# Optimization experiments

Measured on AMD Instinct MI355X. Metric: run time of the kernel, lower is better.

## Reference

```python
import jax, jax.numpy as jnp
import numpy as np

N_NODES = 50000
N_EDGES = 800000
IN_DIM = 64
EDGE_DIM = 32
OUT_DIM = 64
HID = IN_DIM + EDGE_DIM  # repo MLP defaults hidden width = layer input width


def setup_inputs() -> dict:
    key = jax.random.key(0)
    ks = jax.random.split(key, 7)
    x = jax.random.normal(ks[0], (N_NODES, IN_DIM), dtype=jnp.float32)
    edge_index = jax.random.randint(ks[1], (2, N_EDGES), 0, N_NODES, dtype=jnp.int64)
    edge_attr = jax.random.normal(ks[2], (N_EDGES, EDGE_DIM), dtype=jnp.float32)
    s1 = 1.0 / np.sqrt(HID)
    s2 = 1.0 / np.sqrt(HID)
    W1 = jax.random.normal(ks[3], (HID, HID), dtype=jnp.float32) * s1
    b1 = jnp.zeros((HID,), dtype=jnp.float32)
    W2 = jax.random.normal(ks[4], (HID, OUT_DIM), dtype=jnp.float32) * s2
    b2 = jnp.zeros((OUT_DIM,), dtype=jnp.float32)
    return {"x": x, "edge_index": edge_index, "edge_attr": edge_attr,
            "W1": W1, "b1": b1, "W2": W2, "b2": b2}


def reference(x, edge_index, edge_attr, W1, b1, W2, b2):
    row, col = edge_index[0], edge_index[1]
    n_nodes = x.shape[0]
    # gather source node features and fuse with edge features: [E, IN+EDGE]
    h = jnp.concatenate([x[row], edge_attr], axis=1)
    # MLP: one hidden layer with ReLU, linear output
    h = jax.nn.relu(h @ W1 + b1)
    h = h @ W2 + b2  # [E, OUT_DIM]
    # scatter_mean over destination (col) indices
    summed = jax.ops.segment_sum(h, col, num_segments=n_nodes)  # [N, OUT_DIM]
    counts = jax.ops.segment_sum(jnp.ones((h.shape[0],), dtype=h.dtype), col,
                                 num_segments=n_nodes)
    return summed / jnp.maximum(counts, 1.0)[:, None]
```

## Files before the change

### kernel.cpp

```cpp
#include <hip/hip_runtime.h>

#define N_EDGES  800000
#define N_NODES  50000
#define IN_DIM   64
#define EDGE_DIM 32
#define HID      96
#define OUT_DIM  64
#define BE       128
#define PAD      104
#define NTILES   (N_EDGES / BE)
#define THREADS  512
#define GRID     512
#define SCAN_B   1024
#define SCAN_NB  ((N_NODES + SCAN_B - 1) / SCAN_B)

typedef __attribute__((ext_vector_type(8))) short  short8;
typedef __attribute__((ext_vector_type(4))) ushort bf16x4;
typedef __attribute__((ext_vector_type(4))) float  f32x4;

__device__ inline ushort f2bf(float f) {
    union { float f; unsigned u; } v; v.f = f;
    unsigned r = v.u + 0x7FFFu + ((v.u >> 16) & 1u);
    return (ushort)(r >> 16);
}
__device__ inline float b2f(ushort u) {
    union { unsigned u; float f; } v; v.u = ((unsigned)u) << 16;
    return v.f;
}

__global__ __launch_bounds__(256) void hist_kernel(const int* __restrict__ ei,
                                                   int* __restrict__ hist) {
    int e = blockIdx.x * 256 + threadIdx.x;
    if (e < N_EDGES) atomicAdd(&hist[ei[N_EDGES + e]], 1);
}

__global__ __launch_bounds__(SCAN_B) void scan1_kernel(const int* __restrict__ hist,
                                                       int* __restrict__ starts,
                                                       int* __restrict__ bsums) {
    __shared__ int buf[2][SCAN_B];
    const int tid = threadIdx.x;
    const int gid = blockIdx.x * SCAN_B + tid;
    int v = (gid < N_NODES) ? hist[gid] : 0;
    int cur = 0;
    buf[0][tid] = v;
    __syncthreads();
    #pragma unroll
    for (int off = 1; off < SCAN_B; off <<= 1) {
        int t = buf[cur][tid] + ((tid >= off) ? buf[cur][tid - off] : 0);
        buf[cur ^ 1][tid] = t;
        __syncthreads();
        cur ^= 1;
    }
    int incl = buf[cur][tid];
    if (gid < N_NODES) starts[gid] = incl;
    if (tid == SCAN_B - 1) bsums[blockIdx.x] = incl;
}

__global__ __launch_bounds__(SCAN_B) void scan3_kernel(const int* __restrict__ hist,
                                                       int* __restrict__ starts,
                                                       int* __restrict__ cursor,
                                                       const int* __restrict__ bsums) {
    __shared__ int s_off;
    if (threadIdx.x < 64) {
        int v = ((int)threadIdx.x < (int)blockIdx.x) ? bsums[threadIdx.x] : 0;
        #pragma unroll
        for (int o = 32; o >= 1; o >>= 1) v += __shfl_xor(v, o, 64);
        if (threadIdx.x == 0) s_off = v;
    }
    __syncthreads();
    const int gid = blockIdx.x * SCAN_B + threadIdx.x;
    if (gid < N_NODES) {
        int e = starts[gid] - hist[gid] + s_off;
        starts[gid] = e;
        cursor[gid] = e;
    }
}

__global__ __launch_bounds__(256) void fill_kernel(const int* __restrict__ ei,
                                                   int* __restrict__ cursor,
                                                   int* __restrict__ epos) {
    int e = blockIdx.x * 256 + threadIdx.x;
    if (e < N_EDGES) {
        int c = ei[N_EDGES + e];
        int p = atomicAdd(&cursor[c], 1);
        epos[e] = p;
    }
}

__global__ __launch_bounds__(256) void zero_kernel(float* __restrict__ out,
                                                   float* __restrict__ cnt) {
    int i = blockIdx.x * 256 + threadIdx.x;
    if (i < N_NODES * OUT_DIM) out[i] = 0.0f;
    if (i < N_NODES) cnt[i] = 0.0f;
}

__global__ __launch_bounds__(256) void div_kernel(float* __restrict__ out,
                                                  const float* __restrict__ cnt) {
    int i = blockIdx.x * 256 + threadIdx.x;
    if (i < N_NODES * OUT_DIM) {
        float c = cnt[i / OUT_DIM];
        out[i] = out[i] / fmaxf(c, 1.0f);
    }
}

template <bool ATOMIC>
__global__ __launch_bounds__(THREADS, 4) void edge_mlp_mfma_kernel(
    const float* __restrict__ x,
    const int*   __restrict__ ei,
    const float* __restrict__ ea,
    const float* __restrict__ W1,
    const float* __restrict__ b1,
    const float* __restrict__ W2,
    const float* __restrict__ b2,
    float*       __restrict__ out,
    float*       __restrict__ cnt,
    ushort*      __restrict__ temp,
    const int*   __restrict__ epos)
{
    __shared__ ushort sA[BE][PAD];
    __shared__ ushort sW1T[HID][PAD];
    __shared__ ushort sW2T[OUT_DIM][PAD];

    const int tid  = threadIdx.x;
    const int wave = tid >> 6;
    const int lane = tid & 63;
    const int lr   = lane & 15;
    const int lg   = lane >> 4;
    const int el_base = wave * 16;
    const int el   = el_base + (lane >> 2);
    const int part = lane & 3;

    #pragma unroll 2
    for (int i = tid; i < HID * HID / 4; i += THREADS) {
        float4 v = reinterpret_cast<const float4*>(W1)[i];
        int k = (i * 4) / HID, n = (i * 4) % HID;
        sW1T[n + 0][k] = f2bf(v.x); sW1T[n + 1][k] = f2bf(v.y);
        sW1T[n + 2][k] = f2bf(v.z); sW1T[n + 3][k] = f2bf(v.w);
    }
    #pragma unroll 2
    for (int i = tid; i < HID * OUT_DIM / 4; i += THREADS) {
        float4 v = reinterpret_cast<const float4*>(W2)[i];
        int k = (i * 4) / OUT_DIM, n = (i * 4) % OUT_DIM;
        sW2T[n + 0][k] = f2bf(v.x); sW2T[n + 1][k] = f2bf(v.y);
        sW2T[n + 2][k] = f2bf(v.z); sW2T[n + 3][k] = f2bf(v.w);
    }
    float rb1[6], rb2[4];
    #pragma unroll
    for (int nt = 0; nt < 6; ++nt) rb1[nt] = b1[nt * 16 + lr];
    #pragma unroll
    for (int nt = 0; nt < 4; ++nt) rb2[nt] = b2[nt * 16 + lr];
    __syncthreads();

    float4 px0, px1, px2, px3, pe0, pe1;
    int ppos = 0, pdst = 0;
    int tl = blockIdx.x;
    {
        const int e = tl * BE + el;
        const int src = ei[e];
        if constexpr (ATOMIC) pdst = ei[N_EDGES + e];
        else                  ppos = epos[e];
        const float4* xp = reinterpret_cast<const float4*>(x) + (size_t)src * 16;
        const float4* ep = reinterpret_cast<const float4*>(ea) + (size_t)e * 8;
        px0 = xp[part]; px1 = xp[part + 4]; px2 = xp[part + 8]; px3 = xp[part + 12];
        pe0 = ep[part]; pe1 = ep[part + 4];
    }

    for (; tl < NTILES; tl += GRID) {
        {
            bf16x4 w;
            w = bf16x4{ f2bf(px0.x), f2bf(px0.y), f2bf(px0.z), f2bf(px0.w) };
            *(bf16x4*)&sA[el][(part +  0) * 4] = w;
            w = bf16x4{ f2bf(px1.x), f2bf(px1.y), f2bf(px1.z), f2bf(px1.w) };
            *(bf16x4*)&sA[el][(part +  4) * 4] = w;
            w = bf16x4{ f2bf(px2.x), f2bf(px2.y), f2bf(px2.z), f2bf(px2.w) };
            *(bf16x4*)&sA[el][(part +  8) * 4] = w;
            w = bf16x4{ f2bf(px3.x), f2bf(px3.y), f2bf(px3.z), f2bf(px3.w) };
            *(bf16x4*)&sA[el][(part + 12) * 4] = w;
            w = bf16x4{ f2bf(pe0.x), f2bf(pe0.y), f2bf(pe0.z), f2bf(pe0.w) };
            *(bf16x4*)&sA[el][(part + 16) * 4] = w;
            w = bf16x4{ f2bf(pe1.x), f2bf(pe1.y), f2bf(pe1.z), f2bf(pe1.w) };
            *(bf16x4*)&sA[el][(part + 20) * 4] = w;
        }
        const int cpos = ppos, cdst = pdst;
        if constexpr (ATOMIC) {
            if (part == 0) atomicAdd(cnt + cdst, 1.0f);
        }

        const int tn = tl + GRID;
        const bool have = (tn < NTILES);
        float4 nx0, nx1, nx2, nx3, ne0, ne1;
        int npos = 0, ndst = 0;
        if (have) {
            const int e = tn * BE + el;
            const int src = ei[e];
            if constexpr (ATOMIC) ndst = ei[N_EDGES + e];
            else                  npos = epos[e];
            const float4* xp = reinterpret_cast<const float4*>(x) + (size_t)src * 16;
            const float4* ep = reinterpret_cast<const float4*>(ea) + (size_t)e * 8;
            nx0 = xp[part]; nx1 = xp[part + 4]; nx2 = xp[part + 8]; nx3 = xp[part + 12];
            ne0 = ep[part]; ne1 = ep[part + 4];
        }

        asm volatile("s_waitcnt lgkmcnt(0)" ::: "memory");
        __builtin_amdgcn_sched_barrier(0);

        short8 af[3];
        #pragma unroll
        for (int ks = 0; ks < 3; ++ks)
            af[ks] = *(const short8*)&sA[el_base + lr][ks * 32 + lg * 8];

        f32x4 acc1[6];
        #pragma unroll
        for (int nt = 0; nt < 6; ++nt) {
            float bv = rb1[nt];
            acc1[nt] = f32x4{ bv, bv, bv, bv };
        }
        #pragma unroll
        for (int nt = 0; nt < 6; ++nt) {
            short8 bf[3];
            #pragma unroll
            for (int ks = 0; ks < 3; ++ks)
                bf[ks] = *(const short8*)&sW1T[nt * 16 + lr][ks * 32 + lg * 8];
            #pragma unroll
            for (int ks = 0; ks < 3; ++ks)
                acc1[nt] = __builtin_amdgcn_mfma_f32_16x16x32_bf16(
                    af[ks], bf[ks], acc1[nt], 0, 0, 0);
        }

        #pragma unroll
        for (int nt = 0; nt < 6; ++nt)
            #pragma unroll
            for (int j = 0; j < 4; ++j)
                sA[el_base + lg * 4 + j][nt * 16 + lr] =
                    f2bf(fmaxf(acc1[nt][j], 0.0f));
        asm volatile("s_waitcnt lgkmcnt(0)" ::: "memory");
        __builtin_amdgcn_sched_barrier(0);

        short8 a2[3];
        #pragma unroll
        for (int ks = 0; ks < 3; ++ks)
            a2[ks] = *(const short8*)&sA[el_base + lr][ks * 32 + lg * 8];

        f32x4 acc2[4];
        #pragma unroll
        for (int nt = 0; nt < 4; ++nt) {
            float bv = rb2[nt];
            acc2[nt] = f32x4{ bv, bv, bv, bv };
        }
        #pragma unroll
        for (int nt = 0; nt < 4; ++nt) {
            short8 bf[3];
            #pragma unroll
            for (int ks = 0; ks < 3; ++ks)
                bf[ks] = *(const short8*)&sW2T[nt * 16 + lr][ks * 32 + lg * 8];
            #pragma unroll
            for (int ks = 0; ks < 3; ++ks)
                acc2[nt] = __builtin_amdgcn_mfma_f32_16x16x32_bf16(
                    a2[ks], bf[ks], acc2[nt], 0, 0, 0);
        }

        if constexpr (ATOMIC) {
            int nd[4];
            #pragma unroll
            for (int j = 0; j < 4; ++j)
                nd[j] = ei[N_EDGES + tl * BE + el_base + lg * 4 + j];
            #pragma unroll
            for (int nt = 0; nt < 4; ++nt)
                #pragma unroll
                for (int j = 0; j < 4; ++j)
                    atomicAdd(out + (size_t)nd[j] * OUT_DIM + nt * 16 + lr,
                              acc2[nt][j]);
        } else {
            #pragma unroll
            for (int nt = 0; nt < 4; ++nt)
                #pragma unroll
                for (int j = 0; j < 4; ++j)
                    sA[el_base + lg * 4 + j][nt * 16 + lr] = f2bf(acc2[nt][j]);
            asm volatile("s_waitcnt lgkmcnt(0)" ::: "memory");
            __builtin_amdgcn_sched_barrier(0);
            ushort* dst = temp + (size_t)cpos * OUT_DIM + part * 16;
            short8 v0 = *(const short8*)&sA[el][part * 16];
            short8 v1 = *(const short8*)&sA[el][part * 16 + 8];
            *(short8*)dst = v0;
            *(short8*)(dst + 8) = v1;
        }

        if (have) {
            px0 = nx0; px1 = nx1; px2 = nx2; px3 = nx3;
            pe0 = ne0; pe1 = ne1;
            ppos = npos; pdst = ndst;
        }
    }
}

__global__ __launch_bounds__(256) void pull_kernel(const ushort* __restrict__ temp,
                                                   const int* __restrict__ starts,
                                                   const int* __restrict__ hist,
                                                   float* __restrict__ out) {
    const int wave = threadIdx.x >> 6;
    const int lane = threadIdx.x & 63;
    const int node = blockIdx.x * 4 + wave;
    if (node >= N_NODES) return;
    const int deg = hist[node];
    const int st  = starts[node];
    const int r   = lane >> 4;
    const int g   = lane & 15;
    float sx = 0.f, sy = 0.f, sz = 0.f, sw = 0.f;
    const uint2* base = reinterpret_cast<const uint2*>(temp) + (size_t)st * 16 + g;
    for (int i = r; i < deg; i += 4) {
        uint2 u = base[(size_t)i * 16];
        sx += b2f((ushort)(u.x & 0xFFFFu));
        sy += b2f((ushort)(u.x >> 16));
        sz += b2f((ushort)(u.y & 0xFFFFu));
        sw += b2f((ushort)(u.y >> 16));
    }
    #pragma unroll
    for (int o = 16; o <= 32; o <<= 1) {
        sx += __shfl_xor(sx, o, 64);
        sy += __shfl_xor(sy, o, 64);
        sz += __shfl_xor(sz, o, 64);
        sw += __shfl_xor(sw, o, 64);
    }
    if (r == 0) {
        float inv = 1.0f / fmaxf((float)deg, 1.0f);
        float4 o4 = { sx * inv, sy * inv, sz * inv, sw * inv };
        *reinterpret_cast<float4*>(out + (size_t)node * OUT_DIM + g * 4) = o4;
    }
}

extern "C" void kernel_launch(void* const* d_in, const int* in_sizes, int n_in,
                              void* d_out, int out_size, void* d_ws, size_t ws_size,
                              hipStream_t stream) {
    const float* x  = (const float*)d_in[0];
    const int*   ei = (const int*)d_in[1];
    const float* ea = (const float*)d_in[2];
    const float* W1 = (const float*)d_in[3];
    const float* b1 = (const float*)d_in[4];
    const float* W2 = (const float*)d_in[5];
    const float* b2 = (const float*)d_in[6];
    float* out = (float*)d_out;

    char* ws = (char*)d_ws;
    const size_t tempB    = (size_t)N_EDGES * OUT_DIM * sizeof(ushort);
    const size_t eposOff  = tempB;
    const size_t histOff  = eposOff + (size_t)N_EDGES * 4;
    const size_t strOff   = histOff + (size_t)N_NODES * 4;
    const size_t curOff   = strOff + (size_t)N_NODES * 4;
    const size_t bsumOff  = curOff + (size_t)N_NODES * 4;
    const size_t need     = bsumOff + 64 * 4;

    if (ws_size >= need) {
        ushort* temp  = (ushort*)ws;
        int* epos     = (int*)(ws + eposOff);
        int* hist     = (int*)(ws + histOff);
        int* starts   = (int*)(ws + strOff);
        int* cursor   = (int*)(ws + curOff);
        int* bsums    = (int*)(ws + bsumOff);

        hipMemsetAsync(hist, 0, (size_t)N_NODES * 4, stream);
        hist_kernel<<<N_EDGES / 256, 256, 0, stream>>>(ei, hist);
        scan1_kernel<<<SCAN_NB, SCAN_B, 0, stream>>>(hist, starts, bsums);
        scan3_kernel<<<SCAN_NB, SCAN_B, 0, stream>>>(hist, starts, cursor, bsums);
        fill_kernel<<<N_EDGES / 256, 256, 0, stream>>>(ei, cursor, epos);
        edge_mlp_mfma_kernel<false><<<GRID, THREADS, 0, stream>>>(
            x, ei, ea, W1, b1, W2, b2, out, nullptr, temp, epos);
        pull_kernel<<<(N_NODES + 3) / 4, 256, 0, stream>>>(temp, starts, hist, out);
    } else {
        float* cnt = (float*)d_ws;
        zero_kernel<<<(N_NODES * OUT_DIM + 255) / 256, 256, 0, stream>>>(out, cnt);
        edge_mlp_mfma_kernel<true><<<GRID, THREADS, 0, stream>>>(
            x, ei, ea, W1, b1, W2, b2, out, cnt, nullptr, nullptr);
        div_kernel<<<(N_NODES * OUT_DIM + 255) / 256, 256, 0, stream>>>(out, cnt);
    }
}
```

Measured before the change: 174.3 us.

## Load MFMA A-fragments straight from global and keep W2 fragments in registers

Each lane now gathers its own edge's x and edge_attr values directly in the MFMA A-fragment layout, converts them to bf16 in registers, and skips the LDS staging round-trip. The software prefetch of the next tile is dropped. The W2 B-fragments are hoisted out of the tile loop into registers so they are not reloaded from LDS every tile. In exchange it loses the global-load/compute overlap from the prefetch, accepts less coalesced per-lane gathers, and adds register pressure that may reduce occupancy.

```diff
diff --git a/kernel.cpp b/kernel.cpp
--- a/kernel.cpp
+++ b/kernel.cpp
@@ -151,63 +151,35 @@
     for (int nt = 0; nt < 4; ++nt) rb2[nt] = b2[nt * 16 + lr];
     __syncthreads();
 
-    float4 px0, px1, px2, px3, pe0, pe1;
-    int ppos = 0, pdst = 0;
-    int tl = blockIdx.x;
-    {
-        const int e = tl * BE + el;
-        const int src = ei[e];
-        if constexpr (ATOMIC) pdst = ei[N_EDGES + e];
-        else                  ppos = epos[e];
-        const float4* xp = reinterpret_cast<const float4*>(x) + (size_t)src * 16;
-        const float4* ep = reinterpret_cast<const float4*>(ea) + (size_t)e * 8;
-        px0 = xp[part]; px1 = xp[part + 4]; px2 = xp[part + 8]; px3 = xp[part + 12];
-        pe0 = ep[part]; pe1 = ep[part + 4];
-    }
-
-    for (; tl < NTILES; tl += GRID) {
+    short8 bw2[4][3];
+    #pragma unroll
+    for (int nt = 0; nt < 4; ++nt)
+        #pragma unroll
+        for (int ks = 0; ks < 3; ++ks)
+            bw2[nt][ks] = *(const short8*)&sW2T[nt * 16 + lr][ks * 32 + lg * 8];
+
+    for (int tl = blockIdx.x; tl < NTILES; tl += GRID) {
+        const int e0 = tl * BE;
+
+        const int erow = e0 + el_base + lr;
+        const int src  = ei[erow];
+        short8 af[3];
         {
-            bf16x4 w;
-            w = bf16x4{ f2bf(px0.x), f2bf(px0.y), f2bf(px0.z), f2bf(px0.w) };
-            *(bf16x4*)&sA[el][(part +  0) * 4] = w;
-            w = bf16x4{ f2bf(px1.x), f2bf(px1.y), f2bf(px1.z), f2bf(px1.w) };
-            *(bf16x4*)&sA[el][(part +  4) * 4] = w;
-            w = bf16x4{ f2bf(px2.x), f2bf(px2.y), f2bf(px2.z), f2bf(px2.w) };
-            *(bf16x4*)&sA[el][(part +  8) * 4] = w;
-            w = bf16x4{ f2bf(px3.x), f2bf(px3.y), f2bf(px3.z), f2bf(px3.w) };
-            *(bf16x4*)&sA[el][(part + 12) * 4] = w;
-            w = bf16x4{ f2bf(pe0.x), f2bf(pe0.y), f2bf(pe0.z), f2bf(pe0.w) };
-            *(bf16x4*)&sA[el][(part + 16) * 4] = w;
-            w = bf16x4{ f2bf(pe1.x), f2bf(pe1.y), f2bf(pe1.z), f2bf(pe1.w) };
-            *(bf16x4*)&sA[el][(part + 20) * 4] = w;
-        }
-        const int cpos = ppos, cdst = pdst;
+            const float4* xp = reinterpret_cast<const float4*>(x) + (size_t)src * 16;
+            const float4* ep = reinterpret_cast<const float4*>(ea) + (size_t)erow * 8;
+            float4 a0 = xp[lg * 2],     a1 = xp[lg * 2 + 1];
+            float4 b0 = xp[8 + lg * 2], b1v = xp[8 + lg * 2 + 1];
+            float4 c0 = ep[lg * 2],     c1 = ep[lg * 2 + 1];
+            af[0] = short8{ (short)f2bf(a0.x), (short)f2bf(a0.y), (short)f2bf(a0.z), (short)f2bf(a0.w),
+                            (short)f2bf(a1.x), (short)f2bf(a1.y), (short)f2bf(a1.z), (short)f2bf(a1.w) };
+            af[1] = short8{ (short)f2bf(b0.x), (short)f2bf(b0.y), (short)f2bf(b0.z), (short)f2bf(b0.w),
+                            (short)f2bf(b1v.x), (short)f2bf(b1v.y), (short)f2bf(b1v.z), (short)f2bf(b1v.w) };
+            af[2] = short8{ (short)f2bf(c0.x), (short)f2bf(c0.y), (short)f2bf(c0.z), (short)f2bf(c0.w),
+                            (short)f2bf(c1.x), (short)f2bf(c1.y), (short)f2bf(c1.z), (short)f2bf(c1.w) };
+        }
         if constexpr (ATOMIC) {
-            if (part == 0) atomicAdd(cnt + cdst, 1.0f);
-        }
-
-        const int tn = tl + GRID;
-        const bool have = (tn < NTILES);
-        float4 nx0, nx1, nx2, nx3, ne0, ne1;
-        int npos = 0, ndst = 0;
-        if (have) {
-            const int e = tn * BE + el;
-            const int src = ei[e];
-            if constexpr (ATOMIC) ndst = ei[N_EDGES + e];
-            else                  npos = epos[e];
-            const float4* xp = reinterpret_cast<const float4*>(x) + (size_t)src * 16;
-            const float4* ep = reinterpret_cast<const float4*>(ea) + (size_t)e * 8;
-            nx0 = xp[part]; nx1 = xp[part + 4]; nx2 = xp[part + 8]; nx3 = xp[part + 12];
-            ne0 = ep[part]; ne1 = ep[part + 4];
-        }
-
-        asm volatile("s_waitcnt lgkmcnt(0)" ::: "memory");
-        __builtin_amdgcn_sched_barrier(0);
-
-        short8 af[3];
-        #pragma unroll
-        for (int ks = 0; ks < 3; ++ks)
-            af[ks] = *(const short8*)&sA[el_base + lr][ks * 32 + lg * 8];
+            if (lg == 0) atomicAdd(cnt + ei[N_EDGES + erow], 1.0f);
+        }
 
         f32x4 acc1[6];
         #pragma unroll
@@ -248,22 +220,17 @@
             acc2[nt] = f32x4{ bv, bv, bv, bv };
         }
         #pragma unroll
-        for (int nt = 0; nt < 4; ++nt) {
-            short8 bf[3];
-            #pragma unroll
-            for (int ks = 0; ks < 3; ++ks)
-                bf[ks] = *(const short8*)&sW2T[nt * 16 + lr][ks * 32 + lg * 8];
+        for (int nt = 0; nt < 4; ++nt)
             #pragma unroll
             for (int ks = 0; ks < 3; ++ks)
                 acc2[nt] = __builtin_amdgcn_mfma_f32_16x16x32_bf16(
-                    a2[ks], bf[ks], acc2[nt], 0, 0, 0);
-        }
+                    a2[ks], bw2[nt][ks], acc2[nt], 0, 0, 0);
 
         if constexpr (ATOMIC) {
             int nd[4];
             #pragma unroll
             for (int j = 0; j < 4; ++j)
-                nd[j] = ei[N_EDGES + tl * BE + el_base + lg * 4 + j];
+                nd[j] = ei[N_EDGES + e0 + el_base + lg * 4 + j];
             #pragma unroll
             for (int nt = 0; nt < 4; ++nt)
                 #pragma unroll
@@ -278,17 +245,12 @@
                     sA[el_base + lg * 4 + j][nt * 16 + lr] = f2bf(acc2[nt][j]);
             asm volatile("s_waitcnt lgkmcnt(0)" ::: "memory");
             __builtin_amdgcn_sched_barrier(0);
+            const int cpos = epos[e0 + el];
             ushort* dst = temp + (size_t)cpos * OUT_DIM + part * 16;
             short8 v0 = *(const short8*)&sA[el][part * 16];
             short8 v1 = *(const short8*)&sA[el][part * 16 + 8];
             *(short8*)dst = v0;
             *(short8*)(dst + 8) = v1;
-        }
-
-        if (have) {
-            px0 = nx0; px1 = nx1; px2 = nx2; px3 = nx3;
-            pe0 = ne0; pe1 = ne1;
-            ppos = npos; pdst = ndst;
         }
     }
 }
```

Measured after the change: 207.5 us. 1.19x slower.
